# Kernel optimization log

Measured on AMD Instinct MI355X. Metric: run time of the kernel, lower is better.

## Reference

```python
import jax, jax.numpy as jnp
import numpy as np

B, S, D, U = 32, 2048, 1024, 1024


def setup_inputs() -> dict:
    key = jax.random.key(0)
    ks = jax.random.split(key, 10)
    s = 0.02
    return {
        "dec_hidden": jax.random.normal(ks[0], (B, D), jnp.float32),
        "enc_output": jax.random.normal(ks[1], (B, S, D), jnp.float32),
        "enc_pad_mask": jnp.ones((B, S), jnp.int32),  # accepted but unused, as in the original
        "use_coverage": True,
        "prev_coverage": jax.random.uniform(ks[2], (B, S, 1), jnp.float32),
        "Ws_w": jax.random.normal(ks[3], (D, U), jnp.float32) * s,
        "Ws_b": jnp.zeros((U,), jnp.float32),
        "Wh_w": jax.random.normal(ks[4], (D, U), jnp.float32) * s,
        "Wh_b": jnp.zeros((U,), jnp.float32),
        "Wc_w": jax.random.normal(ks[5], (1, U), jnp.float32) * s,
        "Wc_b": jnp.zeros((U,), jnp.float32),
        "V_w": jax.random.normal(ks[6], (U, 1), jnp.float32) * s,
        "V_b": jnp.zeros((1,), jnp.float32),
    }


def reference(dec_hidden, enc_output, enc_pad_mask, use_coverage, prev_coverage,
              Ws_w, Ws_b, Wh_w, Wh_b, Wc_w, Wc_b, V_w, V_b):
    # W_h(dec_hidden) with time axis: [B, 1, U]
    h = (dec_hidden @ Wh_w + Wh_b)[:, None, :]
    # W_s(enc_output): [B, S, U]
    feat = jnp.einsum('bsd,du->bsu', enc_output, Ws_w) + Ws_b + h
    if use_coverage and prev_coverage is not None:
        # W_c(prev_coverage): [B, S, 1] @ [1, U] -> [B, S, U]
        feat = feat + prev_coverage @ Wc_w + Wc_b
        score = jnp.tanh(feat) @ V_w + V_b            # [B, S, 1]
        attention_weights = jax.nn.softmax(score, axis=1)
        coverage = attention_weights + prev_coverage
    else:
        score = jnp.tanh(feat) @ V_w + V_b
        attention_weights = jax.nn.softmax(score, axis=1)
        coverage = attention_weights if use_coverage else []
    # weighted sum over sequence axis: [B, D]
    context_vector = jnp.sum(attention_weights * enc_output, axis=1)
    return context_vector, jnp.squeeze(attention_weights, -1), coverage
```

## Files before the change

kernel.cpp:

```cpp
#include <hip/hip_runtime.h>
#include <hip/hip_bf16.h>

namespace {

constexpr int kB = 32;
constexpr int kS = 2048;
constexpr int kD = 1024;
constexpr int kU = 1024;
constexpr int BM = 128;
constexpr int BN = 128;
constexpr int BK = 64;
constexpr int kMT = (kB * kS) / BM;
constexpr int kNT = kU / BN;
constexpr int kKS = kD / BK;
constexpr size_t kChunk = (size_t)BM * BK * 2;

typedef __attribute__((ext_vector_type(8))) short bf16x8;
typedef __attribute__((ext_vector_type(4))) float f32x4;

__device__ __forceinline__ unsigned short f2bf(float x) {
  union { __hip_bfloat16 h; unsigned short u; } c;
  c.h = __float2bfloat16(x);
  return c.u;
}

__device__ __forceinline__ float tanh_fast(float x) {
  float e = __expf(2.0f * x);
  return 1.0f - 2.0f * __builtin_amdgcn_rcpf(e + 1.0f);
}

__device__ __forceinline__ void gload16(const void* g, void* l) {
  __builtin_amdgcn_global_load_lds(
      (const __attribute__((address_space(1))) void*)g,
      (__attribute__((address_space(3))) void*)l, 16, 0, 0);
}


__global__ __launch_bounds__(256) void h2_kernel(
    const float* __restrict__ dec, const float* __restrict__ Whw,
    const float* __restrict__ Whb, const float* __restrict__ Wsb,
    const float* __restrict__ Wcb, float* __restrict__ h2) {
  const int b = blockIdx.y;
  const int u = blockIdx.x * 256 + threadIdx.x;
  float acc = Whb[u] + Wsb[u] + Wcb[u];
  const float* dh = dec + b * kD;
  #pragma unroll 8
  for (int d = 0; d < kD; ++d) acc += dh[d] * Whw[(size_t)d * kU + u];
  h2[b * kU + u] = acc;
}

__global__ __launch_bounds__(256) void context_kernel(
    const float* __restrict__ enc, const float* __restrict__ attn,
    float* __restrict__ ctx) {
  const int b = blockIdx.z;
  const int s0 = blockIdx.y * 256;
  const int d = blockIdx.x * 256 + threadIdx.x;
  const float* e = enc + ((size_t)b * kS + s0) * kD + d;
  const float* a = attn + (size_t)b * kS + s0;
  float acc = 0.f;
  #pragma unroll 8
  for (int s = 0; s < 256; ++s) acc += a[s] * e[(size_t)s * kD];
  atomicAdd(&ctx[b * kD + d], acc);
}


__global__ __launch_bounds__(256) void convA_kernel(
    const float* __restrict__ enc, unsigned char* __restrict__ encT) {
  const size_t e = ((size_t)blockIdx.x * 256 + threadIdx.x) * 8;
  const int r = (int)(e >> 10), d0 = (int)(e & 1023);
  float4 v0 = *(const float4*)(enc + e);
  float4 v1 = *(const float4*)(enc + e + 4);
  uint4 p;
  p.x = (unsigned)f2bf(v0.x) | ((unsigned)f2bf(v0.y) << 16);
  p.y = (unsigned)f2bf(v0.z) | ((unsigned)f2bf(v0.w) << 16);
  p.z = (unsigned)f2bf(v1.x) | ((unsigned)f2bf(v1.y) << 16);
  p.w = (unsigned)f2bf(v1.z) | ((unsigned)f2bf(v1.w) << 16);
  const int mt = r >> 7, row = r & 127, ks = d0 >> 6, c = d0 & 63;
  unsigned char* dst = encT + ((size_t)mt * kKS + ks) * kChunk + row * 128 +
                       (((c >> 3) << 4) ^ ((row & 7) << 4));
  *(uint4*)dst = p;
}

__global__ __launch_bounds__(256) void tpose2_kernel(
    const float* __restrict__ W, unsigned char* __restrict__ Bt) {
  __shared__ float tile[32][33];
  const int u0 = blockIdx.x * 32, d0 = blockIdx.y * 32;
  const int tx = threadIdx.x, ty = threadIdx.y;
  #pragma unroll
  for (int i = 0; i < 4; ++i)
    tile[ty + i * 8][tx] = W[(size_t)(d0 + ty + i * 8) * kU + u0 + tx];
  __syncthreads();
  #pragma unroll
  for (int i = 0; i < 4; ++i) {
    const int u = u0 + ty + i * 8, d = d0 + tx;
    const int nt = u >> 7, n = u & 127, ks = d >> 6, c = d & 63;
    *(unsigned short*)(Bt + ((size_t)nt * kKS + ks) * kChunk + n * 128 +
                       ((((c >> 3) << 4) ^ ((n & 7) << 4)) + (c & 7) * 2)) =
        f2bf(tile[tx][ty + i * 8]);
  }
}

__global__ __launch_bounds__(256, 4) void score_gemm2_kernel(
    const unsigned char* __restrict__ encT, const unsigned char* __restrict__ Bt,
    const float* __restrict__ h2, const float* __restrict__ pc,
    const float* __restrict__ Wcw, const float* __restrict__ Vw,
    float* __restrict__ scorep) {
  __shared__ __attribute__((aligned(16))) unsigned char smA[kChunk];
  __shared__ __attribute__((aligned(16))) unsigned char smB[kChunk];

  const int tid = threadIdx.x;
  const int lane = tid & 63;
  const int w = tid >> 6;
  const int wr = w >> 1, wc = w & 1;

  const int work = (blockIdx.x & 7) * (kMT * kNT / 8) + (blockIdx.x >> 3);
  const int mtile = work >> 3, ntile = work & 7;
  const int r0 = mtile * BM, n0 = ntile * BN;

  const unsigned char* Ab = encT + (size_t)mtile * kKS * kChunk + (size_t)w * 4096 + lane * 16;
  const unsigned char* Bb = Bt + (size_t)ntile * kKS * kChunk + (size_t)w * 4096 + lane * 16;

  f32x4 acc[4][4];
  #pragma unroll
  for (int i = 0; i < 4; ++i)
    #pragma unroll
    for (int j = 0; j < 4; ++j) acc[i][j] = (f32x4){0.f, 0.f, 0.f, 0.f};

  const int lr = lane & 15, lq = lane >> 4;

  for (int ks = 0; ks < kKS; ++ks) {
    #pragma unroll
    for (int i = 0; i < 4; ++i) {
      gload16(Ab + (size_t)ks * kChunk + i * 1024, smA + w * 4096 + i * 1024);
      gload16(Bb + (size_t)ks * kChunk + i * 1024, smB + w * 4096 + i * 1024);
    }
    __syncthreads();
    #pragma unroll
    for (int k2 = 0; k2 < 2; ++k2) {
      const int kb = k2 * 64 + lq * 16;
      bf16x8 af[4], bfr[4];
      #pragma unroll
      for (int fm = 0; fm < 4; ++fm) {
        const int row = wr * 64 + fm * 16 + lr;
        af[fm] = *(const bf16x8*)(smA + row * 128 + (kb ^ ((row & 7) << 4)));
      }
      #pragma unroll
      for (int fn = 0; fn < 4; ++fn) {
        const int n = wc * 64 + fn * 16 + lr;
        bfr[fn] = *(const bf16x8*)(smB + n * 128 + (kb ^ ((n & 7) << 4)));
      }
      #pragma unroll
      for (int fm = 0; fm < 4; ++fm)
        #pragma unroll
        for (int fn = 0; fn < 4; ++fn)
          acc[fm][fn] =
              __builtin_amdgcn_mfma_f32_16x16x32_bf16(af[fm], bfr[fn], acc[fm][fn], 0, 0, 0);
    }
    __syncthreads();
  }

  const int bidx = r0 >> 11;
  float hv[4], wv[4], vv[4];
  #pragma unroll
  for (int fn = 0; fn < 4; ++fn) {
    const int u = n0 + wc * 64 + fn * 16 + lr;
    hv[fn] = h2[bidx * kU + u];
    wv[fn] = Wcw[u];
    vv[fn] = Vw[u];
  }
  float* plane = scorep + (size_t)((ntile << 1) | wc) * (kB * kS);
  #pragma unroll
  for (int fm = 0; fm < 4; ++fm) {
    #pragma unroll
    for (int j = 0; j < 4; ++j) {
      const int r = r0 + wr * 64 + fm * 16 + lq * 4 + j;
      const float pcv = pc[r];
      float partial = 0.f;
      #pragma unroll
      for (int fn = 0; fn < 4; ++fn) {
        const float feat = acc[fm][fn][j] + hv[fn] + pcv * wv[fn];
        partial += tanh_fast(feat) * vv[fn];
      }
      partial += __shfl_xor(partial, 1);
      partial += __shfl_xor(partial, 2);
      partial += __shfl_xor(partial, 4);
      partial += __shfl_xor(partial, 8);
      if (lr == 0) plane[r] = partial;
    }
  }
}

__global__ __launch_bounds__(256) void softmax2_kernel(
    const float* __restrict__ scorep, const float* __restrict__ pc,
    float* __restrict__ attn, float* __restrict__ cov) {
  const int b = blockIdx.x, tid = threadIdx.x;
  const int lane = tid & 63, wid = tid >> 6;
  const size_t base = (size_t)b * kS + tid * 8;
  float v[8] = {0.f, 0.f, 0.f, 0.f, 0.f, 0.f, 0.f, 0.f};
  #pragma unroll
  for (int p = 0; p < 16; ++p) {
    const float* s = scorep + (size_t)p * (kB * kS) + base;
    float4 a = *(const float4*)(s);
    float4 c = *(const float4*)(s + 4);
    v[0] += a.x; v[1] += a.y; v[2] += a.z; v[3] += a.w;
    v[4] += c.x; v[5] += c.y; v[6] += c.z; v[7] += c.w;
  }
  float m = v[0];
  #pragma unroll
  for (int i = 1; i < 8; ++i) m = fmaxf(m, v[i]);
  #pragma unroll
  for (int msk = 1; msk < 64; msk <<= 1) m = fmaxf(m, __shfl_xor(m, msk));
  __shared__ float redm[4], reds[4];
  if (lane == 0) redm[wid] = m;
  __syncthreads();
  m = fmaxf(fmaxf(redm[0], redm[1]), fmaxf(redm[2], redm[3]));
  float e[8], sum = 0.f;
  #pragma unroll
  for (int i = 0; i < 8; ++i) { e[i] = __expf(v[i] - m); sum += e[i]; }
  #pragma unroll
  for (int msk = 1; msk < 64; msk <<= 1) sum += __shfl_xor(sum, msk);
  if (lane == 0) reds[wid] = sum;
  __syncthreads();
  sum = reds[0] + reds[1] + reds[2] + reds[3];
  const float inv = 1.0f / sum;
  float pv[8], a[8], c[8];
  const float* p = pc + base;
  *(float4*)(pv) = *(const float4*)(p);
  *(float4*)(pv + 4) = *(const float4*)(p + 4);
  #pragma unroll
  for (int i = 0; i < 8; ++i) { a[i] = e[i] * inv; c[i] = a[i] + pv[i]; }
  *(float4*)(attn + base) = *(float4*)(a);
  *(float4*)(attn + base + 4) = *(float4*)(a + 4);
  *(float4*)(cov + base) = *(float4*)(c);
  *(float4*)(cov + base + 4) = *(float4*)(c + 4);
}


__global__ __launch_bounds__(256) void tpose_fb_kernel(
    const float* __restrict__ W, unsigned short* __restrict__ out) {
  __shared__ float tile[32][33];
  const int u0 = blockIdx.x * 32, d0 = blockIdx.y * 32;
  const int tx = threadIdx.x, ty = threadIdx.y;
  #pragma unroll
  for (int i = 0; i < 4; ++i)
    tile[ty + i * 8][tx] = W[(size_t)(d0 + ty + i * 8) * kU + u0 + tx];
  __syncthreads();
  #pragma unroll
  for (int i = 0; i < 4; ++i)
    out[(size_t)(u0 + ty + i * 8) * kD + d0 + tx] = f2bf(tile[tx][ty + i * 8]);
}

__global__ __launch_bounds__(256, 2) void score_gemm_fb_kernel(
    const float* __restrict__ enc, const unsigned short* __restrict__ WsT,
    const float* __restrict__ h2, const float* __restrict__ pc,
    const float* __restrict__ Wcw, const float* __restrict__ Vw,
    float* __restrict__ score) {
  __shared__ __attribute__((aligned(16))) unsigned char smA[BM * BK * 2];
  __shared__ __attribute__((aligned(16))) unsigned char smB[BN * BK * 2];
  const int tid = threadIdx.x;
  const int lane = tid & 63;
  const int wid = tid >> 6;
  const int wr = wid >> 1, wc = wid & 1;
  const int mtile = blockIdx.x >> 3, ntile = blockIdx.x & 7;
  const int r0 = mtile * BM, n0 = ntile * BN;
  f32x4 acc[4][4];
  #pragma unroll
  for (int i = 0; i < 4; ++i)
    #pragma unroll
    for (int j = 0; j < 4; ++j) acc[i][j] = (f32x4){0.f, 0.f, 0.f, 0.f};
  const int kqA = tid & 15;
  const int rowA = tid >> 4;
  const int kcB = tid & 7;
  const int nB = tid >> 3;
  float4 aReg[8];
  uint4 bReg[4];
  #pragma unroll
  for (int i = 0; i < 8; ++i)
    aReg[i] = *(const float4*)(enc + (size_t)(r0 + rowA + 16 * i) * kD + kqA * 4);
  #pragma unroll
  for (int i = 0; i < 4; ++i)
    bReg[i] = *(const uint4*)(WsT + (size_t)(n0 + nB + 32 * i) * kD + kcB * 8);
  const int lr = lane & 15, lq = lane >> 4;
  for (int k0 = 0; k0 < kD; k0 += BK) {
    #pragma unroll
    for (int i = 0; i < 8; ++i) {
      const int row = rowA + 16 * i;
      uint2 p;
      p.x = (unsigned)f2bf(aReg[i].x) | ((unsigned)f2bf(aReg[i].y) << 16);
      p.y = (unsigned)f2bf(aReg[i].z) | ((unsigned)f2bf(aReg[i].w) << 16);
      *(uint2*)(smA + row * 128 + ((kqA * 8) ^ ((row & 7) << 4))) = p;
    }
    #pragma unroll
    for (int i = 0; i < 4; ++i) {
      const int n = nB + 32 * i;
      *(uint4*)(smB + n * 128 + ((kcB * 16) ^ ((n & 7) << 4))) = bReg[i];
    }
    __syncthreads();
    if (k0 + BK < kD) {
      const int kn = k0 + BK;
      #pragma unroll
      for (int i = 0; i < 8; ++i)
        aReg[i] = *(const float4*)(enc + (size_t)(r0 + rowA + 16 * i) * kD + kn + kqA * 4);
      #pragma unroll
      for (int i = 0; i < 4; ++i)
        bReg[i] = *(const uint4*)(WsT + (size_t)(n0 + nB + 32 * i) * kD + kn + kcB * 8);
    }
    #pragma unroll
    for (int ks = 0; ks < 2; ++ks) {
      const int kb = ks * 64 + lq * 16;
      bf16x8 af[4], bfr[4];
      #pragma unroll
      for (int fm = 0; fm < 4; ++fm) {
        const int row = wr * 64 + fm * 16 + lr;
        af[fm] = *(const bf16x8*)(smA + row * 128 + (kb ^ ((row & 7) << 4)));
      }
      #pragma unroll
      for (int fn = 0; fn < 4; ++fn) {
        const int n = wc * 64 + fn * 16 + lr;
        bfr[fn] = *(const bf16x8*)(smB + n * 128 + (kb ^ ((n & 7) << 4)));
      }
      #pragma unroll
      for (int fm = 0; fm < 4; ++fm)
        #pragma unroll
        for (int fn = 0; fn < 4; ++fn)
          acc[fm][fn] =
              __builtin_amdgcn_mfma_f32_16x16x32_bf16(af[fm], bfr[fn], acc[fm][fn], 0, 0, 0);
    }
    __syncthreads();
  }
  const int bidx = r0 >> 11;
  float hv[4], wv[4], vv[4];
  #pragma unroll
  for (int fn = 0; fn < 4; ++fn) {
    const int u = n0 + wc * 64 + fn * 16 + lr;
    hv[fn] = h2[bidx * kU + u];
    wv[fn] = Wcw[u];
    vv[fn] = Vw[u];
  }
  #pragma unroll
  for (int fm = 0; fm < 4; ++fm) {
    #pragma unroll
    for (int j = 0; j < 4; ++j) {
      const int r = r0 + wr * 64 + fm * 16 + lq * 4 + j;
      const float pcv = pc[r];
      float partial = 0.f;
      #pragma unroll
      for (int fn = 0; fn < 4; ++fn) {
        const float feat = acc[fm][fn][j] + hv[fn] + pcv * wv[fn];
        partial += tanh_fast(feat) * vv[fn];
      }
      partial += __shfl_xor(partial, 1);
      partial += __shfl_xor(partial, 2);
      partial += __shfl_xor(partial, 4);
      partial += __shfl_xor(partial, 8);
      if (lr == 0) atomicAdd(&score[r], partial);
    }
  }
}

__global__ __launch_bounds__(256) void softmax_fb_kernel(
    const float* __restrict__ score, const float* __restrict__ pc,
    float* __restrict__ attn, float* __restrict__ cov) {
  const int b = blockIdx.x, tid = threadIdx.x;
  const int lane = tid & 63, wid = tid >> 6;
  const float* s = score + (size_t)b * kS;
  float v[8];
  *(float4*)(v) = *(const float4*)(s + tid * 8);
  *(float4*)(v + 4) = *(const float4*)(s + tid * 8 + 4);
  float m = v[0];
  #pragma unroll
  for (int i = 1; i < 8; ++i) m = fmaxf(m, v[i]);
  #pragma unroll
  for (int msk = 1; msk < 64; msk <<= 1) m = fmaxf(m, __shfl_xor(m, msk));
  __shared__ float redm[4], reds[4];
  if (lane == 0) redm[wid] = m;
  __syncthreads();
  m = fmaxf(fmaxf(redm[0], redm[1]), fmaxf(redm[2], redm[3]));
  float e[8], sum = 0.f;
  #pragma unroll
  for (int i = 0; i < 8; ++i) { e[i] = __expf(v[i] - m); sum += e[i]; }
  #pragma unroll
  for (int msk = 1; msk < 64; msk <<= 1) sum += __shfl_xor(sum, msk);
  if (lane == 0) reds[wid] = sum;
  __syncthreads();
  sum = reds[0] + reds[1] + reds[2] + reds[3];
  const float inv = 1.0f / sum;
  float pv[8], a[8], c[8];
  const float* p = pc + (size_t)b * kS + tid * 8;
  *(float4*)(pv) = *(const float4*)(p);
  *(float4*)(pv + 4) = *(const float4*)(p + 4);
  #pragma unroll
  for (int i = 0; i < 8; ++i) { a[i] = e[i] * inv; c[i] = a[i] + pv[i]; }
  *(float4*)(attn + (size_t)b * kS + tid * 8) = *(float4*)(a);
  *(float4*)(attn + (size_t)b * kS + tid * 8 + 4) = *(float4*)(a + 4);
  *(float4*)(cov + (size_t)b * kS + tid * 8) = *(float4*)(c);
  *(float4*)(cov + (size_t)b * kS + tid * 8 + 4) = *(float4*)(c + 4);
}

}

extern "C" void kernel_launch(void* const* d_in, const int* in_sizes, int n_in,
                              void* d_out, int out_size, void* d_ws, size_t ws_size,
                              hipStream_t stream) {
  (void)in_sizes; (void)n_in; (void)out_size;
  const float* dec = (const float*)d_in[0];
  const float* enc = (const float*)d_in[1];
  const float* pc  = (const float*)d_in[4];
  const float* Wsw = (const float*)d_in[5];
  const float* Wsb = (const float*)d_in[6];
  const float* Whw = (const float*)d_in[7];
  const float* Whb = (const float*)d_in[8];
  const float* Wcw = (const float*)d_in[9];
  const float* Wcb = (const float*)d_in[10];
  const float* Vw  = (const float*)d_in[11];

  float* ctx  = (float*)d_out;
  float* attn = (float*)d_out + kB * kD;
  float* cov  = attn + kB * kS;

  unsigned char* ws = (unsigned char*)d_ws;

  const size_t encT_sz  = (size_t)kB * kS * kD * 2;
  const size_t Bt_sz    = (size_t)kU * kD * 2;
  const size_t h2_sz    = (size_t)kB * kU * 4;
  const size_t sp_sz    = (size_t)16 * kB * kS * 4;
  const size_t need     = encT_sz + Bt_sz + h2_sz + sp_sz;

  hipMemsetAsync(ctx, 0, kB * kD * sizeof(float), stream);

  if (ws_size >= need) {
    unsigned char* encT = ws;
    unsigned char* Bt   = ws + encT_sz;
    float* h2     = (float*)(ws + encT_sz + Bt_sz);
    float* scorep = (float*)(ws + encT_sz + Bt_sz + h2_sz);

    convA_kernel<<<dim3((kB * kS * kD / 8) / 256), 256, 0, stream>>>(enc, encT);
    tpose2_kernel<<<dim3(kU / 32, kD / 32), dim3(32, 8), 0, stream>>>(Wsw, Bt);
    h2_kernel<<<dim3(kU / 256, kB), 256, 0, stream>>>(dec, Whw, Whb, Wsb, Wcb, h2);
    score_gemm2_kernel<<<dim3(kMT * kNT), 256, 0, stream>>>(
        encT, Bt, h2, pc, Wcw, Vw, scorep);
    softmax2_kernel<<<dim3(kB), 256, 0, stream>>>(scorep, pc, attn, cov);
    context_kernel<<<dim3(kD / 256, kS / 256, kB), 256, 0, stream>>>(enc, attn, ctx);
  } else {
    unsigned short* WsT = (unsigned short*)ws;
    float* h2    = (float*)(ws + (size_t)2 * 1024 * 1024);
    float* score = (float*)(ws + (size_t)2 * 1024 * 1024 + 131072);
    hipMemsetAsync(score, 0, kB * kS * sizeof(float), stream);
    h2_kernel<<<dim3(kU / 256, kB), 256, 0, stream>>>(dec, Whw, Whb, Wsb, Wcb, h2);
    tpose_fb_kernel<<<dim3(kU / 32, kD / 32), dim3(32, 8), 0, stream>>>(Wsw, WsT);
    score_gemm_fb_kernel<<<dim3(kMT * kNT), 256, 0, stream>>>(
        enc, WsT, h2, pc, Wcw, Vw, score);
    softmax_fb_kernel<<<dim3(kB), 256, 0, stream>>>(score, pc, attn, cov);
    context_kernel<<<dim3(kD / 256, kS / 256, kB), 256, 0, stream>>>(enc, attn, ctx);
  }
}
```

Baseline: 347.0 us.

## Use 256x256 double-buffered GEMM tiles and bf16 context reduction without atomics

Moves the score GEMM from 128x128 tiles with 4 waves to 256x256 tiles with 8 waves. It double-buffers LDS (128KB), overlaps global-to-LDS loads with MFMA using explicit waitcnt and barriers, and raises wave priority around the MFMAs. The encoder layout is repacked into 256-row panels to match. The context sum now reads the bf16 encoder copy instead of fp32, reduces in shared memory, and drops the atomics and the ctx memset, halving its input traffic at the cost of bf16 precision in the context vector.

New measurement: 310.6 us. 1.12x faster.

```diff
diff --git a/kernel.cpp b/kernel.cpp
--- a/kernel.cpp
+++ b/kernel.cpp
@@ -7,13 +7,16 @@
 constexpr int kS = 2048;
 constexpr int kD = 1024;
 constexpr int kU = 1024;
-constexpr int BM = 128;
-constexpr int BN = 128;
+
+constexpr int BM = 256;
+constexpr int BN = 256;
 constexpr int BK = 64;
+constexpr int kKT = kD / BK;
 constexpr int kMT = (kB * kS) / BM;
 constexpr int kNT = kU / BN;
-constexpr int kKS = kD / BK;
-constexpr size_t kChunk = (size_t)BM * BK * 2;
+constexpr size_t kHalf = 16384;
+constexpr size_t kTileChunk = 2 * kHalf;
+constexpr size_t kPanel = (size_t)kKT * kTileChunk;
 
 typedef __attribute__((ext_vector_type(8))) short bf16x8;
 typedef __attribute__((ext_vector_type(4))) float f32x4;
@@ -22,6 +25,12 @@
   union { __hip_bfloat16 h; unsigned short u; } c;
   c.h = __float2bfloat16(x);
   return c.u;
+}
+
+__device__ __forceinline__ float bf2f(unsigned short u) {
+  union { unsigned int i; float f; } c;
+  c.i = ((unsigned int)u) << 16;
+  return c.f;
 }
 
 __device__ __forceinline__ float tanh_fast(float x) {
@@ -49,7 +58,509 @@
   h2[b * kU + u] = acc;
 }
 
-__global__ __launch_bounds__(256) void context_kernel(
+
+__global__ __launch_bounds__(256) void convA_kernel(
+    const float* __restrict__ enc, unsigned char* __restrict__ encT) {
+  const size_t e = ((size_t)blockIdx.x * 256 + threadIdx.x) * 8;
+  const int r = (int)(e >> 10), d0 = (int)(e & 1023);
+  float4 v0 = *(const float4*)(enc + e);
+  float4 v1 = *(const float4*)(enc + e + 4);
+  uint4 p;
+  p.x = (unsigned)f2bf(v0.x) | ((unsigned)f2bf(v0.y) << 16);
+  p.y = (unsigned)f2bf(v0.z) | ((unsigned)f2bf(v0.w) << 16);
+  p.z = (unsigned)f2bf(v1.x) | ((unsigned)f2bf(v1.y) << 16);
+  p.w = (unsigned)f2bf(v1.z) | ((unsigned)f2bf(v1.w) << 16);
+  const int mt = r >> 8, rh = (r >> 7) & 1, row = r & 127;
+  const int kt = d0 >> 6, c8 = (d0 & 63) >> 3;
+  unsigned char* dst = encT + (size_t)mt * kPanel + (size_t)kt * kTileChunk +
+                       (size_t)rh * kHalf + row * 128 +
+                       (((unsigned)c8 << 4) ^ (((unsigned)row & 7) << 4));
+  *(uint4*)dst = p;
+}
+
+__global__ __launch_bounds__(256) void tpose2_kernel(
+    const float* __restrict__ W, unsigned char* __restrict__ Bt) {
+  __shared__ float tile[32][33];
+  const int u0 = blockIdx.x * 32, d0 = blockIdx.y * 32;
+  const int tx = threadIdx.x, ty = threadIdx.y;
+  #pragma unroll
+  for (int i = 0; i < 4; ++i)
+    tile[ty + i * 8][tx] = W[(size_t)(d0 + ty + i * 8) * kU + u0 + tx];
+  __syncthreads();
+  #pragma unroll
+  for (int i = 0; i < 4; ++i) {
+    const int u = u0 + ty + i * 8, d = d0 + tx;
+    const int nt = u >> 8, gh = (u >> 7) & 1, n = u & 127;
+    const int kt = d >> 6, c = d & 63;
+    *(unsigned short*)(Bt + (size_t)nt * kPanel + (size_t)kt * kTileChunk +
+                       (size_t)gh * kHalf + n * 128 +
+                       (((((unsigned)c >> 3) << 4) ^ (((unsigned)n & 7) << 4)) +
+                        (c & 7) * 2)) = f2bf(tile[tx][ty + i * 8]);
+  }
+}
+
+#define MFMA_BF16(a, b, c) __builtin_amdgcn_mfma_f32_16x16x32_bf16((a), (b), (c), 0, 0, 0)
+
+__global__ __launch_bounds__(512, 2) void score_gemm3_kernel(
+    const unsigned char* __restrict__ encT, const unsigned char* __restrict__ Bt,
+    const float* __restrict__ h2, const float* __restrict__ pc,
+    const float* __restrict__ Wcw, const float* __restrict__ Vw,
+    float* __restrict__ scorep) {
+  __shared__ __attribute__((aligned(16))) unsigned char lds[131072];
+
+  const int tid = threadIdx.x;
+  const int lane = tid & 63;
+  const int w = tid >> 6;
+  const int lr = lane & 15, lq = lane >> 4;
+  const int wrow = (w >> 2) * 64;
+  const int wcs = w & 3;
+  const int bg = wcs >> 1;
+  const int wncol = (wcs & 1) * 64;
+
+  const int work = (blockIdx.x & 7) * 128 + (blockIdx.x >> 3);
+  const int mtile = work >> 2, ntile = work & 3;
+
+  const unsigned char* Ab = encT + (size_t)mtile * kPanel;
+  const unsigned char* Bb = Bt + (size_t)ntile * kPanel;
+  const int so0 = tid * 16;
+  const int so1 = tid * 16 + 8192;
+
+  f32x4 acc[2][4][4];
+  #pragma unroll
+  for (int h = 0; h < 2; ++h)
+    #pragma unroll
+    for (int i = 0; i < 4; ++i)
+      #pragma unroll
+      for (int j = 0; j < 4; ++j) acc[h][i][j] = (f32x4){0.f, 0.f, 0.f, 0.f};
+
+  {
+    const unsigned char* At = Ab;
+    const unsigned char* Btt = Bb;
+    gload16(At + so0, lds + 0 + so0);
+    gload16(At + so1, lds + 0 + so1);
+    gload16(Btt + so0, lds + 65536 + so0);
+    gload16(Btt + so1, lds + 65536 + so1);
+    gload16(Btt + kHalf + so0, lds + 65536 + kHalf + so0);
+    gload16(Btt + kHalf + so1, lds + 65536 + kHalf + so1);
+    gload16(At + kHalf + so0, lds + kHalf + so0);
+    gload16(At + kHalf + so1, lds + kHalf + so1);
+  }
+
+  for (int t = 0; t < kKT - 1; ++t) {
+    const int p = t & 1;
+    const int aP = p * 2 * (int)kHalf;
+    const int aQ = (1 - p) * 2 * (int)kHalf;
+    const int bP = 65536 + p * 2 * (int)kHalf;
+    const int bQ = 65536 + (1 - p) * 2 * (int)kHalf;
+    const unsigned char* An = Ab + (size_t)(t + 1) * kTileChunk;
+    const unsigned char* Bn = Bb + (size_t)(t + 1) * kTileChunk;
+
+    gload16(An + so0, lds + aQ + so0);
+    gload16(An + so1, lds + aQ + so1);
+    gload16(Bn + so0, lds + bQ + so0);
+    gload16(Bn + so1, lds + bQ + so1);
+    gload16(Bn + (int)kHalf + so0, lds + bQ + (int)kHalf + so0);
+    gload16(Bn + (int)kHalf + so1, lds + bQ + (int)kHalf + so1);
+    asm volatile("s_waitcnt vmcnt(8)" ::: "memory");
+    __builtin_amdgcn_s_barrier();
+    __builtin_amdgcn_sched_barrier(0);
+
+    bf16x8 bfr[4][2];
+    #pragma unroll
+    for (int cf = 0; cf < 4; ++cf)
+      #pragma unroll
+      for (int ks = 0; ks < 2; ++ks) {
+        const int n = wncol + cf * 16 + lr;
+        bfr[cf][ks] = *(const bf16x8*)(lds + bP + bg * (int)kHalf + n * 128 +
+                                       ((ks * 64 + lq * 16) ^ ((n & 7) << 4)));
+      }
+    #pragma unroll
+    for (int ks = 0; ks < 2; ++ks) {
+      bf16x8 af[4];
+      #pragma unroll
+      for (int rf = 0; rf < 4; ++rf) {
+        const int row = wrow + rf * 16 + lr;
+        af[rf] = *(const bf16x8*)(lds + aP + row * 128 +
+                                  ((ks * 64 + lq * 16) ^ ((row & 7) << 4)));
+      }
+      __builtin_amdgcn_s_setprio(1);
+      #pragma unroll
+      for (int rf = 0; rf < 4; ++rf)
+        #pragma unroll
+        for (int cf = 0; cf < 4; ++cf)
+          acc[0][rf][cf] = MFMA_BF16(af[rf], bfr[cf][ks], acc[0][rf][cf]);
+      __builtin_amdgcn_s_setprio(0);
+    }
+
+    gload16(An + (int)kHalf + so0, lds + aQ + (int)kHalf + so0);
+    gload16(An + (int)kHalf + so1, lds + aQ + (int)kHalf + so1);
+    asm volatile("s_waitcnt vmcnt(8)" ::: "memory");
+    __builtin_amdgcn_s_barrier();
+    __builtin_amdgcn_sched_barrier(0);
+
+    #pragma unroll
+    for (int ks = 0; ks < 2; ++ks) {
+      bf16x8 af[4];
+      #pragma unroll
+      for (int rf = 0; rf < 4; ++rf) {
+        const int row = wrow + rf * 16 + lr;
+        af[rf] = *(const bf16x8*)(lds + aP + (int)kHalf + row * 128 +
+                                  ((ks * 64 + lq * 16) ^ ((row & 7) << 4)));
+      }
+      __builtin_amdgcn_s_setprio(1);
+      #pragma unroll
+      for (int rf = 0; rf < 4; ++rf)
+        #pragma unroll
+        for (int cf = 0; cf < 4; ++cf)
+          acc[1][rf][cf] = MFMA_BF16(af[rf], bfr[cf][ks], acc[1][rf][cf]);
+      __builtin_amdgcn_s_setprio(0);
+    }
+  }
+
+  {
+    const int p = (kKT - 1) & 1;
+    const int aP = p * 2 * (int)kHalf;
+    const int bP = 65536 + p * 2 * (int)kHalf;
+
+    asm volatile("s_waitcnt vmcnt(2)" ::: "memory");
+    __builtin_amdgcn_s_barrier();
+    __builtin_amdgcn_sched_barrier(0);
+
+    bf16x8 bfr[4][2];
+    #pragma unroll
+    for (int cf = 0; cf < 4; ++cf)
+      #pragma unroll
+      for (int ks = 0; ks < 2; ++ks) {
+        const int n = wncol + cf * 16 + lr;
+        bfr[cf][ks] = *(const bf16x8*)(lds + bP + bg * (int)kHalf + n * 128 +
+                                       ((ks * 64 + lq * 16) ^ ((n & 7) << 4)));
+      }
+    #pragma unroll
+    for (int ks = 0; ks < 2; ++ks) {
+      bf16x8 af[4];
+      #pragma unroll
+      for (int rf = 0; rf < 4; ++rf) {
+        const int row = wrow + rf * 16 + lr;
+        af[rf] = *(const bf16x8*)(lds + aP + row * 128 +
+                                  ((ks * 64 + lq * 16) ^ ((row & 7) << 4)));
+      }
+      #pragma unroll
+      for (int rf = 0; rf < 4; ++rf)
+        #pragma unroll
+        for (int cf = 0; cf < 4; ++cf)
+          acc[0][rf][cf] = MFMA_BF16(af[rf], bfr[cf][ks], acc[0][rf][cf]);
+    }
+
+    asm volatile("s_waitcnt vmcnt(0)" ::: "memory");
+    __builtin_amdgcn_s_barrier();
+    __builtin_amdgcn_sched_barrier(0);
+
+    #pragma unroll
+    for (int ks = 0; ks < 2; ++ks) {
+      bf16x8 af[4];
+      #pragma unroll
+      for (int rf = 0; rf < 4; ++rf) {
+        const int row = wrow + rf * 16 + lr;
+        af[rf] = *(const bf16x8*)(lds + aP + (int)kHalf + row * 128 +
+                                  ((ks * 64 + lq * 16) ^ ((row & 7) << 4)));
+      }
+      #pragma unroll
+      for (int rf = 0; rf < 4; ++rf)
+        #pragma unroll
+        for (int cf = 0; cf < 4; ++cf)
+          acc[1][rf][cf] = MFMA_BF16(af[rf], bfr[cf][ks], acc[1][rf][cf]);
+    }
+  }
+
+  const int bidx = mtile >> 3;
+  float hv[4], wv[4], vv[4];
+  #pragma unroll
+  for (int cf = 0; cf < 4; ++cf) {
+    const int u = ntile * BN + wcs * 64 + cf * 16 + lr;
+    hv[cf] = h2[bidx * kU + u];
+    wv[cf] = Wcw[u];
+    vv[cf] = Vw[u];
+  }
+  float* plane = scorep + (size_t)(ntile * 4 + wcs) * (kB * kS);
+  #pragma unroll
+  for (int h = 0; h < 2; ++h) {
+    #pragma unroll
+    for (int rf = 0; rf < 4; ++rf) {
+      #pragma unroll
+      for (int j = 0; j < 4; ++j) {
+        const int r = mtile * BM + h * 128 + wrow + rf * 16 + lq * 4 + j;
+        const float pcv = pc[r];
+        float partial = 0.f;
+        #pragma unroll
+        for (int cf = 0; cf < 4; ++cf) {
+          const float feat = acc[h][rf][cf][j] + hv[cf] + pcv * wv[cf];
+          partial += tanh_fast(feat) * vv[cf];
+        }
+        partial += __shfl_xor(partial, 1);
+        partial += __shfl_xor(partial, 2);
+        partial += __shfl_xor(partial, 4);
+        partial += __shfl_xor(partial, 8);
+        if (lr == 0) plane[r] = partial;
+      }
+    }
+  }
+}
+
+__global__ __launch_bounds__(256) void softmax2_kernel(
+    const float* __restrict__ scorep, const float* __restrict__ pc,
+    float* __restrict__ attn, float* __restrict__ cov) {
+  const int b = blockIdx.x, tid = threadIdx.x;
+  const int lane = tid & 63, wid = tid >> 6;
+  const size_t base = (size_t)b * kS + tid * 8;
+  float v[8] = {0.f, 0.f, 0.f, 0.f, 0.f, 0.f, 0.f, 0.f};
+  #pragma unroll
+  for (int p = 0; p < 16; ++p) {
+    const float* s = scorep + (size_t)p * (kB * kS) + base;
+    float4 a = *(const float4*)(s);
+    float4 c = *(const float4*)(s + 4);
+    v[0] += a.x; v[1] += a.y; v[2] += a.z; v[3] += a.w;
+    v[4] += c.x; v[5] += c.y; v[6] += c.z; v[7] += c.w;
+  }
+  float m = v[0];
+  #pragma unroll
+  for (int i = 1; i < 8; ++i) m = fmaxf(m, v[i]);
+  #pragma unroll
+  for (int msk = 1; msk < 64; msk <<= 1) m = fmaxf(m, __shfl_xor(m, msk));
+  __shared__ float redm[4], reds[4];
+  if (lane == 0) redm[wid] = m;
+  __syncthreads();
+  m = fmaxf(fmaxf(redm[0], redm[1]), fmaxf(redm[2], redm[3]));
+  float e[8], sum = 0.f;
+  #pragma unroll
+  for (int i = 0; i < 8; ++i) { e[i] = __expf(v[i] - m); sum += e[i]; }
+  #pragma unroll
+  for (int msk = 1; msk < 64; msk <<= 1) sum += __shfl_xor(sum, msk);
+  if (lane == 0) reds[wid] = sum;
+  __syncthreads();
+  sum = reds[0] + reds[1] + reds[2] + reds[3];
+  const float inv = 1.0f / sum;
+  float pv[8], a[8], c[8];
+  const float* p = pc + base;
+  *(float4*)(pv) = *(const float4*)(p);
+  *(float4*)(pv + 4) = *(const float4*)(p + 4);
+  #pragma unroll
+  for (int i = 0; i < 8; ++i) { a[i] = e[i] * inv; c[i] = a[i] + pv[i]; }
+  *(float4*)(attn + base) = *(float4*)(a);
+  *(float4*)(attn + base + 4) = *(float4*)(a + 4);
+  *(float4*)(cov + base) = *(float4*)(c);
+  *(float4*)(cov + base + 4) = *(float4*)(c + 4);
+}
+
+__global__ __launch_bounds__(256) void context2_kernel(
+    const unsigned char* __restrict__ encT, const float* __restrict__ attn,
+    float* __restrict__ ctx) {
+  const int kt = blockIdx.x;
+  const int b = blockIdx.y;
+  const int cg = threadIdx.x & 7;
+  const int rgrp = threadIdx.x >> 3;
+  float acc8[8];
+  #pragma unroll
+  for (int j = 0; j < 8; ++j) acc8[j] = 0.f;
+  const float* ab = attn + (size_t)b * kS;
+  for (int it = 0; it < kS / 32; ++it) {
+    const int s = it * 32 + rgrp;
+    const int r = b * kS + s;
+    const int mt = r >> 8, rh = (r >> 7) & 1, row = r & 127;
+    const unsigned char* chunk = encT + (size_t)mt * kPanel +
+                                 (size_t)kt * kTileChunk + (size_t)rh * kHalf;
+    uint4 v = *(const uint4*)(chunk + row * 128 +
+                              ((((unsigned)cg << 4) ^ (((unsigned)row & 7) << 4))));
+    const float a = ab[s];
+    const unsigned int* vw = (const unsigned int*)&v;
+    #pragma unroll
+    for (int q = 0; q < 4; ++q) {
+      acc8[2 * q]     += a * bf2f((unsigned short)(vw[q] & 0xffff));
+      acc8[2 * q + 1] += a * bf2f((unsigned short)(vw[q] >> 16));
+    }
+  }
+  __shared__ float red[256 * 8];
+  #pragma unroll
+  for (int j = 0; j < 8; ++j) red[threadIdx.x * 8 + j] = acc8[j];
+  __syncthreads();
+  if (rgrp < 8) {
+  }
+  for (int stride = 16; stride > 0; stride >>= 1) {
+    if (rgrp < stride) {
+      #pragma unroll
+      for (int j = 0; j < 8; ++j)
+        red[(rgrp * 8 + cg) * 8 + j] += red[((rgrp + stride) * 8 + cg) * 8 + j];
+    }
+    __syncthreads();
+  }
+  if (rgrp == 0) {
+    #pragma unroll
+    for (int j = 0; j < 8; ++j)
+      ctx[(size_t)b * kD + kt * 64 + cg * 8 + j] = red[cg * 8 + j];
+  }
+}
+
+
+__global__ __launch_bounds__(256) void tpose_fb_kernel(
+    const float* __restrict__ W, unsigned short* __restrict__ out) {
+  __shared__ float tile[32][33];
+  const int u0 = blockIdx.x * 32, d0 = blockIdx.y * 32;
+  const int tx = threadIdx.x, ty = threadIdx.y;
+  #pragma unroll
+  for (int i = 0; i < 4; ++i)
+    tile[ty + i * 8][tx] = W[(size_t)(d0 + ty + i * 8) * kU + u0 + tx];
+  __syncthreads();
+  #pragma unroll
+  for (int i = 0; i < 4; ++i)
+    out[(size_t)(u0 + ty + i * 8) * kD + d0 + tx] = f2bf(tile[tx][ty + i * 8]);
+}
+
+__global__ __launch_bounds__(256, 2) void score_gemm_fb_kernel(
+    const float* __restrict__ enc, const unsigned short* __restrict__ WsT,
+    const float* __restrict__ h2, const float* __restrict__ pc,
+    const float* __restrict__ Wcw, const float* __restrict__ Vw,
+    float* __restrict__ score) {
+  __shared__ __attribute__((aligned(16))) unsigned char smA[128 * 64 * 2];
+  __shared__ __attribute__((aligned(16))) unsigned char smB[128 * 64 * 2];
+  const int tid = threadIdx.x;
+  const int lane = tid & 63;
+  const int wid = tid >> 6;
+  const int wr = wid >> 1, wc = wid & 1;
+  const int mtile = blockIdx.x >> 3, ntile = blockIdx.x & 7;
+  const int r0 = mtile * 128, n0 = ntile * 128;
+  f32x4 acc[4][4];
+  #pragma unroll
+  for (int i = 0; i < 4; ++i)
+    #pragma unroll
+    for (int j = 0; j < 4; ++j) acc[i][j] = (f32x4){0.f, 0.f, 0.f, 0.f};
+  const int kqA = tid & 15;
+  const int rowA = tid >> 4;
+  const int kcB = tid & 7;
+  const int nB = tid >> 3;
+  float4 aReg[8];
+  uint4 bReg[4];
+  #pragma unroll
+  for (int i = 0; i < 8; ++i)
+    aReg[i] = *(const float4*)(enc + (size_t)(r0 + rowA + 16 * i) * kD + kqA * 4);
+  #pragma unroll
+  for (int i = 0; i < 4; ++i)
+    bReg[i] = *(const uint4*)(WsT + (size_t)(n0 + nB + 32 * i) * kD + kcB * 8);
+  const int lr = lane & 15, lq = lane >> 4;
+  for (int k0 = 0; k0 < kD; k0 += 64) {
+    #pragma unroll
+    for (int i = 0; i < 8; ++i) {
+      const int row = rowA + 16 * i;
+      uint2 p;
+      p.x = (unsigned)f2bf(aReg[i].x) | ((unsigned)f2bf(aReg[i].y) << 16);
+      p.y = (unsigned)f2bf(aReg[i].z) | ((unsigned)f2bf(aReg[i].w) << 16);
+      *(uint2*)(smA + row * 128 + ((kqA * 8) ^ ((row & 7) << 4))) = p;
+    }
+    #pragma unroll
+    for (int i = 0; i < 4; ++i) {
+      const int n = nB + 32 * i;
+      *(uint4*)(smB + n * 128 + ((kcB * 16) ^ ((n & 7) << 4))) = bReg[i];
+    }
+    __syncthreads();
+    if (k0 + 64 < kD) {
+      const int kn = k0 + 64;
+      #pragma unroll
+      for (int i = 0; i < 8; ++i)
+        aReg[i] = *(const float4*)(enc + (size_t)(r0 + rowA + 16 * i) * kD + kn + kqA * 4);
+      #pragma unroll
+      for (int i = 0; i < 4; ++i)
+        bReg[i] = *(const uint4*)(WsT + (size_t)(n0 + nB + 32 * i) * kD + kn + kcB * 8);
+    }
+    #pragma unroll
+    for (int ks = 0; ks < 2; ++ks) {
+      const int kb = ks * 64 + lq * 16;
+      bf16x8 af[4], bfr[4];
+      #pragma unroll
+      for (int fm = 0; fm < 4; ++fm) {
+        const int row = wr * 64 + fm * 16 + lr;
+        af[fm] = *(const bf16x8*)(smA + row * 128 + (kb ^ ((row & 7) << 4)));
+      }
+      #pragma unroll
+      for (int fn = 0; fn < 4; ++fn) {
+        const int n = wc * 64 + fn * 16 + lr;
+        bfr[fn] = *(const bf16x8*)(smB + n * 128 + (kb ^ ((n & 7) << 4)));
+      }
+      #pragma unroll
+      for (int fm = 0; fm < 4; ++fm)
+        #pragma unroll
+        for (int fn = 0; fn < 4; ++fn)
+          acc[fm][fn] = MFMA_BF16(af[fm], bfr[fn], acc[fm][fn]);
+    }
+    __syncthreads();
+  }
+  const int bidx = r0 >> 11;
+  float hv[4], wv[4], vv[4];
+  #pragma unroll
+  for (int fn = 0; fn < 4; ++fn) {
+    const int u = n0 + wc * 64 + fn * 16 + lr;
+    hv[fn] = h2[bidx * kU + u];
+    wv[fn] = Wcw[u];
+    vv[fn] = Vw[u];
+  }
+  #pragma unroll
+  for (int fm = 0; fm < 4; ++fm) {
+    #pragma unroll
+    for (int j = 0; j < 4; ++j) {
+      const int r = r0 + wr * 64 + fm * 16 + lq * 4 + j;
+      const float pcv = pc[r];
+      float partial = 0.f;
+      #pragma unroll
+      for (int fn = 0; fn < 4; ++fn) {
+        const float feat = acc[fm][fn][j] + hv[fn] + pcv * wv[fn];
+        partial += tanh_fast(feat) * vv[fn];
+      }
+      partial += __shfl_xor(partial, 1);
+      partial += __shfl_xor(partial, 2);
+      partial += __shfl_xor(partial, 4);
+      partial += __shfl_xor(partial, 8);
+      if (lr == 0) atomicAdd(&score[r], partial);
+    }
+  }
+}
+
+__global__ __launch_bounds__(256) void softmax_fb_kernel(
+    const float* __restrict__ score, const float* __restrict__ pc,
+    float* __restrict__ attn, float* __restrict__ cov) {
+  const int b = blockIdx.x, tid = threadIdx.x;
+  const int lane = tid & 63, wid = tid >> 6;
+  const float* s = score + (size_t)b * kS;
+  float v[8];
+  *(float4*)(v) = *(const float4*)(s + tid * 8);
+  *(float4*)(v + 4) = *(const float4*)(s + tid * 8 + 4);
+  float m = v[0];
+  #pragma unroll
+  for (int i = 1; i < 8; ++i) m = fmaxf(m, v[i]);
+  #pragma unroll
+  for (int msk = 1; msk < 64; msk <<= 1) m = fmaxf(m, __shfl_xor(m, msk));
+  __shared__ float redm[4], reds[4];
+  if (lane == 0) redm[wid] = m;
+  __syncthreads();
+  m = fmaxf(fmaxf(redm[0], redm[1]), fmaxf(redm[2], redm[3]));
+  float e[8], sum = 0.f;
+  #pragma unroll
+  for (int i = 0; i < 8; ++i) { e[i] = __expf(v[i] - m); sum += e[i]; }
+  #pragma unroll
+  for (int msk = 1; msk < 64; msk <<= 1) sum += __shfl_xor(sum, msk);
+  if (lane == 0) reds[wid] = sum;
+  __syncthreads();
+  sum = reds[0] + reds[1] + reds[2] + reds[3];
+  const float inv = 1.0f / sum;
+  float pv[8], a[8], c[8];
+  const float* p = pc + (size_t)b * kS + tid * 8;
+  *(float4*)(pv) = *(const float4*)(p);
+  *(float4*)(pv + 4) = *(const float4*)(p + 4);
+  #pragma unroll
+  for (int i = 0; i < 8; ++i) { a[i] = e[i] * inv; c[i] = a[i] + pv[i]; }
+  *(float4*)(attn + (size_t)b * kS + tid * 8) = *(float4*)(a);
+  *(float4*)(attn + (size_t)b * kS + tid * 8 + 4) = *(float4*)(a + 4);
+  *(float4*)(cov + (size_t)b * kS + tid * 8) = *(float4*)(c);
+  *(float4*)(cov + (size_t)b * kS + tid * 8 + 4) = *(float4*)(c + 4);
+}
+
+__global__ __launch_bounds__(256) void context_fb_kernel(
     const float* __restrict__ enc, const float* __restrict__ attn,
     float* __restrict__ ctx) {
   const int b = blockIdx.z;
@@ -61,340 +572,6 @@
   #pragma unroll 8
   for (int s = 0; s < 256; ++s) acc += a[s] * e[(size_t)s * kD];
   atomicAdd(&ctx[b * kD + d], acc);
-}
-
-
-__global__ __launch_bounds__(256) void convA_kernel(
-    const float* __restrict__ enc, unsigned char* __restrict__ encT) {
-  const size_t e = ((size_t)blockIdx.x * 256 + threadIdx.x) * 8;
-  const int r = (int)(e >> 10), d0 = (int)(e & 1023);
-  float4 v0 = *(const float4*)(enc + e);
-  float4 v1 = *(const float4*)(enc + e + 4);
-  uint4 p;
-  p.x = (unsigned)f2bf(v0.x) | ((unsigned)f2bf(v0.y) << 16);
-  p.y = (unsigned)f2bf(v0.z) | ((unsigned)f2bf(v0.w) << 16);
-  p.z = (unsigned)f2bf(v1.x) | ((unsigned)f2bf(v1.y) << 16);
-  p.w = (unsigned)f2bf(v1.z) | ((unsigned)f2bf(v1.w) << 16);
-  const int mt = r >> 7, row = r & 127, ks = d0 >> 6, c = d0 & 63;
-  unsigned char* dst = encT + ((size_t)mt * kKS + ks) * kChunk + row * 128 +
-                       (((c >> 3) << 4) ^ ((row & 7) << 4));
-  *(uint4*)dst = p;
-}
-
-__global__ __launch_bounds__(256) void tpose2_kernel(
-    const float* __restrict__ W, unsigned char* __restrict__ Bt) {
-  __shared__ float tile[32][33];
-  const int u0 = blockIdx.x * 32, d0 = blockIdx.y * 32;
-  const int tx = threadIdx.x, ty = threadIdx.y;
-  #pragma unroll
-  for (int i = 0; i < 4; ++i)
-    tile[ty + i * 8][tx] = W[(size_t)(d0 + ty + i * 8) * kU + u0 + tx];
-  __syncthreads();
-  #pragma unroll
-  for (int i = 0; i < 4; ++i) {
-    const int u = u0 + ty + i * 8, d = d0 + tx;
-    const int nt = u >> 7, n = u & 127, ks = d >> 6, c = d & 63;
-    *(unsigned short*)(Bt + ((size_t)nt * kKS + ks) * kChunk + n * 128 +
-                       ((((c >> 3) << 4) ^ ((n & 7) << 4)) + (c & 7) * 2)) =
-        f2bf(tile[tx][ty + i * 8]);
-  }
-}
-
-__global__ __launch_bounds__(256, 4) void score_gemm2_kernel(
-    const unsigned char* __restrict__ encT, const unsigned char* __restrict__ Bt,
-    const float* __restrict__ h2, const float* __restrict__ pc,
-    const float* __restrict__ Wcw, const float* __restrict__ Vw,
-    float* __restrict__ scorep) {
-  __shared__ __attribute__((aligned(16))) unsigned char smA[kChunk];
-  __shared__ __attribute__((aligned(16))) unsigned char smB[kChunk];
-
-  const int tid = threadIdx.x;
-  const int lane = tid & 63;
-  const int w = tid >> 6;
-  const int wr = w >> 1, wc = w & 1;
-
-  const int work = (blockIdx.x & 7) * (kMT * kNT / 8) + (blockIdx.x >> 3);
-  const int mtile = work >> 3, ntile = work & 7;
-  const int r0 = mtile * BM, n0 = ntile * BN;
-
-  const unsigned char* Ab = encT + (size_t)mtile * kKS * kChunk + (size_t)w * 4096 + lane * 16;
-  const unsigned char* Bb = Bt + (size_t)ntile * kKS * kChunk + (size_t)w * 4096 + lane * 16;
-
-  f32x4 acc[4][4];
-  #pragma unroll
-  for (int i = 0; i < 4; ++i)
-    #pragma unroll
-    for (int j = 0; j < 4; ++j) acc[i][j] = (f32x4){0.f, 0.f, 0.f, 0.f};
-
-  const int lr = lane & 15, lq = lane >> 4;
-
-  for (int ks = 0; ks < kKS; ++ks) {
-    #pragma unroll
-    for (int i = 0; i < 4; ++i) {
-      gload16(Ab + (size_t)ks * kChunk + i * 1024, smA + w * 4096 + i * 1024);
-      gload16(Bb + (size_t)ks * kChunk + i * 1024, smB + w * 4096 + i * 1024);
-    }
-    __syncthreads();
-    #pragma unroll
-    for (int k2 = 0; k2 < 2; ++k2) {
-      const int kb = k2 * 64 + lq * 16;
-      bf16x8 af[4], bfr[4];
-      #pragma unroll
-      for (int fm = 0; fm < 4; ++fm) {
-        const int row = wr * 64 + fm * 16 + lr;
-        af[fm] = *(const bf16x8*)(smA + row * 128 + (kb ^ ((row & 7) << 4)));
-      }
-      #pragma unroll
-      for (int fn = 0; fn < 4; ++fn) {
-        const int n = wc * 64 + fn * 16 + lr;
-        bfr[fn] = *(const bf16x8*)(smB + n * 128 + (kb ^ ((n & 7) << 4)));
-      }
-      #pragma unroll
-      for (int fm = 0; fm < 4; ++fm)
-        #pragma unroll
-        for (int fn = 0; fn < 4; ++fn)
-          acc[fm][fn] =
-              __builtin_amdgcn_mfma_f32_16x16x32_bf16(af[fm], bfr[fn], acc[fm][fn], 0, 0, 0);
-    }
-    __syncthreads();
-  }
-
-  const int bidx = r0 >> 11;
-  float hv[4], wv[4], vv[4];
-  #pragma unroll
-  for (int fn = 0; fn < 4; ++fn) {
-    const int u = n0 + wc * 64 + fn * 16 + lr;
-    hv[fn] = h2[bidx * kU + u];
-    wv[fn] = Wcw[u];
-    vv[fn] = Vw[u];
-  }
-  float* plane = scorep + (size_t)((ntile << 1) | wc) * (kB * kS);
-  #pragma unroll
-  for (int fm = 0; fm < 4; ++fm) {
-    #pragma unroll
-    for (int j = 0; j < 4; ++j) {
-      const int r = r0 + wr * 64 + fm * 16 + lq * 4 + j;
-      const float pcv = pc[r];
-      float partial = 0.f;
-      #pragma unroll
-      for (int fn = 0; fn < 4; ++fn) {
-        const float feat = acc[fm][fn][j] + hv[fn] + pcv * wv[fn];
-        partial += tanh_fast(feat) * vv[fn];
-      }
-      partial += __shfl_xor(partial, 1);
-      partial += __shfl_xor(partial, 2);
-      partial += __shfl_xor(partial, 4);
-      partial += __shfl_xor(partial, 8);
-      if (lr == 0) plane[r] = partial;
-    }
-  }
-}
-
-__global__ __launch_bounds__(256) void softmax2_kernel(
-    const float* __restrict__ scorep, const float* __restrict__ pc,
-    float* __restrict__ attn, float* __restrict__ cov) {
-  const int b = blockIdx.x, tid = threadIdx.x;
-  const int lane = tid & 63, wid = tid >> 6;
-  const size_t base = (size_t)b * kS + tid * 8;
-  float v[8] = {0.f, 0.f, 0.f, 0.f, 0.f, 0.f, 0.f, 0.f};
-  #pragma unroll
-  for (int p = 0; p < 16; ++p) {
-    const float* s = scorep + (size_t)p * (kB * kS) + base;
-    float4 a = *(const float4*)(s);
-    float4 c = *(const float4*)(s + 4);
-    v[0] += a.x; v[1] += a.y; v[2] += a.z; v[3] += a.w;
-    v[4] += c.x; v[5] += c.y; v[6] += c.z; v[7] += c.w;
-  }
-  float m = v[0];
-  #pragma unroll
-  for (int i = 1; i < 8; ++i) m = fmaxf(m, v[i]);
-  #pragma unroll
-  for (int msk = 1; msk < 64; msk <<= 1) m = fmaxf(m, __shfl_xor(m, msk));
-  __shared__ float redm[4], reds[4];
-  if (lane == 0) redm[wid] = m;
-  __syncthreads();
-  m = fmaxf(fmaxf(redm[0], redm[1]), fmaxf(redm[2], redm[3]));
-  float e[8], sum = 0.f;
-  #pragma unroll
-  for (int i = 0; i < 8; ++i) { e[i] = __expf(v[i] - m); sum += e[i]; }
-  #pragma unroll
-  for (int msk = 1; msk < 64; msk <<= 1) sum += __shfl_xor(sum, msk);
-  if (lane == 0) reds[wid] = sum;
-  __syncthreads();
-  sum = reds[0] + reds[1] + reds[2] + reds[3];
-  const float inv = 1.0f / sum;
-  float pv[8], a[8], c[8];
-  const float* p = pc + base;
-  *(float4*)(pv) = *(const float4*)(p);
-  *(float4*)(pv + 4) = *(const float4*)(p + 4);
-  #pragma unroll
-  for (int i = 0; i < 8; ++i) { a[i] = e[i] * inv; c[i] = a[i] + pv[i]; }
-  *(float4*)(attn + base) = *(float4*)(a);
-  *(float4*)(attn + base + 4) = *(float4*)(a + 4);
-  *(float4*)(cov + base) = *(float4*)(c);
-  *(float4*)(cov + base + 4) = *(float4*)(c + 4);
-}
-
-
-__global__ __launch_bounds__(256) void tpose_fb_kernel(
-    const float* __restrict__ W, unsigned short* __restrict__ out) {
-  __shared__ float tile[32][33];
-  const int u0 = blockIdx.x * 32, d0 = blockIdx.y * 32;
-  const int tx = threadIdx.x, ty = threadIdx.y;
-  #pragma unroll
-  for (int i = 0; i < 4; ++i)
-    tile[ty + i * 8][tx] = W[(size_t)(d0 + ty + i * 8) * kU + u0 + tx];
-  __syncthreads();
-  #pragma unroll
-  for (int i = 0; i < 4; ++i)
-    out[(size_t)(u0 + ty + i * 8) * kD + d0 + tx] = f2bf(tile[tx][ty + i * 8]);
-}
-
-__global__ __launch_bounds__(256, 2) void score_gemm_fb_kernel(
-    const float* __restrict__ enc, const unsigned short* __restrict__ WsT,
-    const float* __restrict__ h2, const float* __restrict__ pc,
-    const float* __restrict__ Wcw, const float* __restrict__ Vw,
-    float* __restrict__ score) {
-  __shared__ __attribute__((aligned(16))) unsigned char smA[BM * BK * 2];
-  __shared__ __attribute__((aligned(16))) unsigned char smB[BN * BK * 2];
-  const int tid = threadIdx.x;
-  const int lane = tid & 63;
-  const int wid = tid >> 6;
-  const int wr = wid >> 1, wc = wid & 1;
-  const int mtile = blockIdx.x >> 3, ntile = blockIdx.x & 7;
-  const int r0 = mtile * BM, n0 = ntile * BN;
-  f32x4 acc[4][4];
-  #pragma unroll
-  for (int i = 0; i < 4; ++i)
-    #pragma unroll
-    for (int j = 0; j < 4; ++j) acc[i][j] = (f32x4){0.f, 0.f, 0.f, 0.f};
-  const int kqA = tid & 15;
-  const int rowA = tid >> 4;
-  const int kcB = tid & 7;
-  const int nB = tid >> 3;
-  float4 aReg[8];
-  uint4 bReg[4];
-  #pragma unroll
-  for (int i = 0; i < 8; ++i)
-    aReg[i] = *(const float4*)(enc + (size_t)(r0 + rowA + 16 * i) * kD + kqA * 4);
-  #pragma unroll
-  for (int i = 0; i < 4; ++i)
-    bReg[i] = *(const uint4*)(WsT + (size_t)(n0 + nB + 32 * i) * kD + kcB * 8);
-  const int lr = lane & 15, lq = lane >> 4;
-  for (int k0 = 0; k0 < kD; k0 += BK) {
-    #pragma unroll
-    for (int i = 0; i < 8; ++i) {
-      const int row = rowA + 16 * i;
-      uint2 p;
-      p.x = (unsigned)f2bf(aReg[i].x) | ((unsigned)f2bf(aReg[i].y) << 16);
-      p.y = (unsigned)f2bf(aReg[i].z) | ((unsigned)f2bf(aReg[i].w) << 16);
-      *(uint2*)(smA + row * 128 + ((kqA * 8) ^ ((row & 7) << 4))) = p;
-    }
-    #pragma unroll
-    for (int i = 0; i < 4; ++i) {
-      const int n = nB + 32 * i;
-      *(uint4*)(smB + n * 128 + ((kcB * 16) ^ ((n & 7) << 4))) = bReg[i];
-    }
-    __syncthreads();
-    if (k0 + BK < kD) {
-      const int kn = k0 + BK;
-      #pragma unroll
-      for (int i = 0; i < 8; ++i)
-        aReg[i] = *(const float4*)(enc + (size_t)(r0 + rowA + 16 * i) * kD + kn + kqA * 4);
-      #pragma unroll
-      for (int i = 0; i < 4; ++i)
-        bReg[i] = *(const uint4*)(WsT + (size_t)(n0 + nB + 32 * i) * kD + kn + kcB * 8);
-    }
-    #pragma unroll
-    for (int ks = 0; ks < 2; ++ks) {
-      const int kb = ks * 64 + lq * 16;
-      bf16x8 af[4], bfr[4];
-      #pragma unroll
-      for (int fm = 0; fm < 4; ++fm) {
-        const int row = wr * 64 + fm * 16 + lr;
-        af[fm] = *(const bf16x8*)(smA + row * 128 + (kb ^ ((row & 7) << 4)));
-      }
-      #pragma unroll
-      for (int fn = 0; fn < 4; ++fn) {
-        const int n = wc * 64 + fn * 16 + lr;
-        bfr[fn] = *(const bf16x8*)(smB + n * 128 + (kb ^ ((n & 7) << 4)));
-      }
-      #pragma unroll
-      for (int fm = 0; fm < 4; ++fm)
-        #pragma unroll
-        for (int fn = 0; fn < 4; ++fn)
-          acc[fm][fn] =
-              __builtin_amdgcn_mfma_f32_16x16x32_bf16(af[fm], bfr[fn], acc[fm][fn], 0, 0, 0);
-    }
-    __syncthreads();
-  }
-  const int bidx = r0 >> 11;
-  float hv[4], wv[4], vv[4];
-  #pragma unroll
-  for (int fn = 0; fn < 4; ++fn) {
-    const int u = n0 + wc * 64 + fn * 16 + lr;
-    hv[fn] = h2[bidx * kU + u];
-    wv[fn] = Wcw[u];
-    vv[fn] = Vw[u];
-  }
-  #pragma unroll
-  for (int fm = 0; fm < 4; ++fm) {
-    #pragma unroll
-    for (int j = 0; j < 4; ++j) {
-      const int r = r0 + wr * 64 + fm * 16 + lq * 4 + j;
-      const float pcv = pc[r];
-      float partial = 0.f;
-      #pragma unroll
-      for (int fn = 0; fn < 4; ++fn) {
-        const float feat = acc[fm][fn][j] + hv[fn] + pcv * wv[fn];
-        partial += tanh_fast(feat) * vv[fn];
-      }
-      partial += __shfl_xor(partial, 1);
-      partial += __shfl_xor(partial, 2);
-      partial += __shfl_xor(partial, 4);
-      partial += __shfl_xor(partial, 8);
-      if (lr == 0) atomicAdd(&score[r], partial);
-    }
-  }
-}
-
-__global__ __launch_bounds__(256) void softmax_fb_kernel(
-    const float* __restrict__ score, const float* __restrict__ pc,
-    float* __restrict__ attn, float* __restrict__ cov) {
-  const int b = blockIdx.x, tid = threadIdx.x;
-  const int lane = tid & 63, wid = tid >> 6;
-  const float* s = score + (size_t)b * kS;
-  float v[8];
-  *(float4*)(v) = *(const float4*)(s + tid * 8);
-  *(float4*)(v + 4) = *(const float4*)(s + tid * 8 + 4);
-  float m = v[0];
-  #pragma unroll
-  for (int i = 1; i < 8; ++i) m = fmaxf(m, v[i]);
-  #pragma unroll
-  for (int msk = 1; msk < 64; msk <<= 1) m = fmaxf(m, __shfl_xor(m, msk));
-  __shared__ float redm[4], reds[4];
-  if (lane == 0) redm[wid] = m;
-  __syncthreads();
-  m = fmaxf(fmaxf(redm[0], redm[1]), fmaxf(redm[2], redm[3]));
-  float e[8], sum = 0.f;
-  #pragma unroll
-  for (int i = 0; i < 8; ++i) { e[i] = __expf(v[i] - m); sum += e[i]; }
-  #pragma unroll
-  for (int msk = 1; msk < 64; msk <<= 1) sum += __shfl_xor(sum, msk);
-  if (lane == 0) reds[wid] = sum;
-  __syncthreads();
-  sum = reds[0] + reds[1] + reds[2] + reds[3];
-  const float inv = 1.0f / sum;
-  float pv[8], a[8], c[8];
-  const float* p = pc + (size_t)b * kS + tid * 8;
-  *(float4*)(pv) = *(const float4*)(p);
-  *(float4*)(pv + 4) = *(const float4*)(p + 4);
-  #pragma unroll
-  for (int i = 0; i < 8; ++i) { a[i] = e[i] * inv; c[i] = a[i] + pv[i]; }
-  *(float4*)(attn + (size_t)b * kS + tid * 8) = *(float4*)(a);
-  *(float4*)(attn + (size_t)b * kS + tid * 8 + 4) = *(float4*)(a + 4);
-  *(float4*)(cov + (size_t)b * kS + tid * 8) = *(float4*)(c);
-  *(float4*)(cov + (size_t)b * kS + tid * 8 + 4) = *(float4*)(c + 4);
 }
 
 }
@@ -420,13 +597,11 @@
 
   unsigned char* ws = (unsigned char*)d_ws;
 
-  const size_t encT_sz  = (size_t)kB * kS * kD * 2;
-  const size_t Bt_sz    = (size_t)kU * kD * 2;
-  const size_t h2_sz    = (size_t)kB * kU * 4;
-  const size_t sp_sz    = (size_t)16 * kB * kS * 4;
-  const size_t need     = encT_sz + Bt_sz + h2_sz + sp_sz;
-
-  hipMemsetAsync(ctx, 0, kB * kD * sizeof(float), stream);
+  const size_t encT_sz = (size_t)kB * kS * kD * 2;
+  const size_t Bt_sz   = (size_t)kU * kD * 2;
+  const size_t h2_sz   = (size_t)kB * kU * 4;
+  const size_t sp_sz   = (size_t)16 * kB * kS * 4;
+  const size_t need    = encT_sz + Bt_sz + h2_sz + sp_sz;
 
   if (ws_size >= need) {
     unsigned char* encT = ws;
@@ -437,20 +612,21 @@
     convA_kernel<<<dim3((kB * kS * kD / 8) / 256), 256, 0, stream>>>(enc, encT);
     tpose2_kernel<<<dim3(kU / 32, kD / 32), dim3(32, 8), 0, stream>>>(Wsw, Bt);
     h2_kernel<<<dim3(kU / 256, kB), 256, 0, stream>>>(dec, Whw, Whb, Wsb, Wcb, h2);
-    score_gemm2_kernel<<<dim3(kMT * kNT), 256, 0, stream>>>(
+    score_gemm3_kernel<<<dim3(kMT * kNT), 512, 0, stream>>>(
         encT, Bt, h2, pc, Wcw, Vw, scorep);
     softmax2_kernel<<<dim3(kB), 256, 0, stream>>>(scorep, pc, attn, cov);
-    context_kernel<<<dim3(kD / 256, kS / 256, kB), 256, 0, stream>>>(enc, attn, ctx);
+    context2_kernel<<<dim3(kD / 64, kB), 256, 0, stream>>>(encT, attn, ctx);
   } else {
     unsigned short* WsT = (unsigned short*)ws;
     float* h2    = (float*)(ws + (size_t)2 * 1024 * 1024);
     float* score = (float*)(ws + (size_t)2 * 1024 * 1024 + 131072);
     hipMemsetAsync(score, 0, kB * kS * sizeof(float), stream);
+    hipMemsetAsync(ctx, 0, kB * kD * sizeof(float), stream);
     h2_kernel<<<dim3(kU / 256, kB), 256, 0, stream>>>(dec, Whw, Whb, Wsb, Wcb, h2);
     tpose_fb_kernel<<<dim3(kU / 32, kD / 32), dim3(32, 8), 0, stream>>>(Wsw, WsT);
-    score_gemm_fb_kernel<<<dim3(kMT * kNT), 256, 0, stream>>>(
+    score_gemm_fb_kernel<<<dim3(4096), 256, 0, stream>>>(
         enc, WsT, h2, pc, Wcw, Vw, score);
     softmax_fb_kernel<<<dim3(kB), 256, 0, stream>>>(score, pc, attn, cov);
-    context_kernel<<<dim3(kD / 256, kS / 256, kB), 256, 0, stream>>>(enc, attn, ctx);
-  }
-}
+    context_fb_kernel<<<dim3(kD / 256, kS / 256, kB), 256, 0, stream>>>(enc, attn, ctx);
+  }
+}
```
